# Performance work log

Measured on AMD Instinct MI355X. Metric: run time of the kernel, lower is better.

## Reference

```python
import jax, jax.numpy as jnp
import numpy as np
from math import ceil

EMBED = 512
HEADS = 8
HD = EMBED // HEADS  # 64
FFN = 2048
MIN_CHUNK = 32
LN_EPS = 1e-5


def layer_norm(x, g, b):
    mu = jnp.mean(x, axis=-1, keepdims=True)
    var = jnp.var(x, axis=-1, keepdims=True)
    return (x - mu) * jax.lax.rsqrt(var + LN_EPS) * g + b


def masked_attention(q, k, v, mask_bool, L):
    # q,k,v: [B*H, L, HD]; mask_bool: [B*H, L] (True = padding)
    BH = q.shape[0]
    S = max(MIN_CHUNK, ceil(L / 4))  # dynamic chunk size (static given L)
    C = ceil(L / S)
    pad = C * S - L
    if pad:
        q = jnp.pad(q, ((0, 0), (0, pad), (0, 0)))
        k = jnp.pad(k, ((0, 0), (0, pad), (0, 0)))
        v = jnp.pad(v, ((0, 0), (0, pad), (0, 0)))
        mask_bool = jnp.pad(mask_bool, ((0, 0), (0, pad)), constant_values=True)
    qc = q.reshape(BH, C, S, HD)
    kc = k.reshape(BH, C, S, HD)
    vc = v.reshape(BH, C, S, HD)
    mc = mask_bool.reshape(BH, C, S)
    # pad one phantom (fully masked) chunk on each side, then gather 3-chunk windows
    kp = jnp.pad(kc, ((0, 0), (1, 1), (0, 0), (0, 0)))
    vp = jnp.pad(vc, ((0, 0), (1, 1), (0, 0), (0, 0)))
    mp = jnp.pad(mc, ((0, 0), (1, 1), (0, 0)), constant_values=True)
    k_win = jnp.concatenate([kp[:, i:i + C] for i in range(3)], axis=2)  # [BH,C,3S,HD]
    v_win = jnp.concatenate([vp[:, i:i + C] for i in range(3)], axis=2)
    m_win = jnp.concatenate([mp[:, i:i + C] for i in range(3)], axis=2)  # [BH,C,3S]
    scores = jnp.einsum('bcqd,bckd->bcqk', qc, k_win) / jnp.sqrt(jnp.float32(HD))
    scores = jnp.where(m_win[:, :, None, :], -jnp.inf, scores)
    w = jax.nn.softmax(scores, axis=-1)
    out = jnp.einsum('bcqk,bckd->bcqd', w, v_win)
    return out.reshape(BH, C * S, HD)[:, :L]


def setup_inputs() -> dict:
    key = jax.random.key(0)
    ks = jax.random.split(key, 6)
    B, L, D = 4, 2048, EMBED
    s = 0.02
    return {
        'x': jax.random.normal(ks[0], (B, L, D), jnp.float32),
        'mask': jnp.zeros((B, L), jnp.int32),
        'qkv_w': jax.random.normal(ks[1], (D, 3 * D), jnp.float32) * s,
        'qkv_b': jnp.zeros((3 * D,), jnp.float32),
        'out_w': jax.random.normal(ks[2], (D, D), jnp.float32) * s,
        'out_b': jnp.zeros((D,), jnp.float32),
        'ffn_w1': jax.random.normal(ks[3], (D, FFN), jnp.float32) * s,
        'ffn_b1': jnp.zeros((FFN,), jnp.float32),
        'ffn_w2': jax.random.normal(ks[4], (FFN, D), jnp.float32) * s,
        'ffn_b2': jnp.zeros((D,), jnp.float32),
        'ln1_g': jnp.ones((D,), jnp.float32),
        'ln1_b': jnp.zeros((D,), jnp.float32),
        'ln2_g': jnp.ones((D,), jnp.float32),
        'ln2_b': jnp.zeros((D,), jnp.float32),
    }


def reference(x, mask, qkv_w, qkv_b, out_w, out_b, ffn_w1, ffn_b1, ffn_w2, ffn_b2, ln1_g, ln1_b, ln2_g, ln2_b):
    B, L, D = x.shape
    qkv = x @ qkv_w + qkv_b
    q, k, v = jnp.split(qkv, 3, axis=-1)

    def to_heads(t):
        return t.reshape(B, L, HEADS, HD).transpose(0, 2, 1, 3).reshape(B * HEADS, L, HD)

    mb = jnp.broadcast_to(mask.astype(bool)[:, None, :], (B, HEADS, L)).reshape(B * HEADS, L)
    a = masked_attention(to_heads(q), to_heads(k), to_heads(v), mb, L)
    a = a.reshape(B, HEADS, L, HD).transpose(0, 2, 1, 3).reshape(B, L, D)
    x = x + (a @ out_w + out_b)  # dropout is identity in eval
    x = layer_norm(x, ln1_g, ln1_b)
    h = jax.nn.gelu(x @ ffn_w1 + ffn_b1, approximate=False) @ ffn_w2 + ffn_b2
    x = layer_norm(x + h, ln2_g, ln2_b)
    return x
```

## Files before the change

### kernel.cpp

```cpp
#include <hip/hip_runtime.h>
#include <hip/hip_bf16.h>
#include <math.h>

#define EMBED 512
#define HEADS 8
#define HD    64
#define FFN_  2048
#define NB    4
#define LSEQ  2048
#define MROWS (NB*LSEQ)
#define BHN   (NB*HEADS)

typedef __attribute__((ext_vector_type(8))) short bf16x8;
typedef __attribute__((ext_vector_type(4))) float f32x4;
#define MFMA16(a,b,c) __builtin_amdgcn_mfma_f32_16x16x32_bf16(a,b,c,0,0,0)

__device__ __forceinline__ unsigned short f2bf(float f) {
    unsigned int u = __float_as_uint(f);
    u += 0x7fff + ((u >> 16) & 1);
    return (unsigned short)(u >> 16);
}
__device__ __forceinline__ unsigned int cvt_pk_bf16(float lo, float hi) {
    unsigned int r;
    asm("v_cvt_pk_bf16_f32 %0, %1, %2" : "=v"(r) : "v"(lo), "v"(hi));
    return r;
}
__device__ __forceinline__ void gl_lds16(const unsigned short* g, unsigned short* l) {
    __builtin_amdgcn_global_load_lds(
        (const __attribute__((address_space(1))) unsigned int*)g,
        (__attribute__((address_space(3))) unsigned int*)l, 16, 0, 0);
}
__device__ __forceinline__ float gelu_f(float v) {
    return 0.5f * v * (1.0f + erff(v * 0.70710678118654752f));
}


__global__ __launch_bounds__(256) void cvt_bf16(const float* __restrict__ in,
                                                unsigned short* __restrict__ out, int n) {
    int i = (blockIdx.x * 256 + threadIdx.x) * 8;
    if (i >= n) return;
    float4 a = *reinterpret_cast<const float4*>(&in[i]);
    float4 b = *reinterpret_cast<const float4*>(&in[i + 4]);
    unsigned short t[8] = {f2bf(a.x), f2bf(a.y), f2bf(a.z), f2bf(a.w),
                           f2bf(b.x), f2bf(b.y), f2bf(b.z), f2bf(b.w)};
    *reinterpret_cast<uint4*>(&out[i]) = *reinterpret_cast<uint4*>(t);
}

__global__ __launch_bounds__(256) void wtrans(const float* __restrict__ in,
                                              unsigned short* __restrict__ out,
                                              int K, int N) {
    __shared__ float tile[32][33];
    const int k0 = blockIdx.y * 32, n0 = blockIdx.x * 32;
    const int t = threadIdx.x;
    const int r = t >> 3, c = (t & 7) * 4;
    float4 v = *reinterpret_cast<const float4*>(&in[(size_t)(k0 + r) * N + n0 + c]);
    tile[r][c] = v.x; tile[r][c + 1] = v.y; tile[r][c + 2] = v.z; tile[r][c + 3] = v.w;
    __syncthreads();
    unsigned short tmp[4] = {f2bf(tile[c + 0][r]), f2bf(tile[c + 1][r]),
                             f2bf(tile[c + 2][r]), f2bf(tile[c + 3][r])};
    *reinterpret_cast<uint2*>(&out[(size_t)(n0 + r) * K + k0 + c]) =
        *reinterpret_cast<uint2*>(tmp);
}

__global__ __launch_bounds__(256) void vtransp(const unsigned short* __restrict__ v,
                                               unsigned short* __restrict__ vT) {
    __shared__ unsigned short tile[64][72];
    const int bh = blockIdx.y, l0 = blockIdx.x * 64;
    const int t = threadIdx.x;
    #pragma unroll
    for (int u = 0; u < 2; ++u) {
        int id = t + u * 256; int r = id >> 3, c = (id & 7) * 8;
        *reinterpret_cast<uint4*>(&tile[r][c]) = *reinterpret_cast<const uint4*>(
            &v[((size_t)bh * LSEQ + l0 + r) * HD + c]);
    }
    __syncthreads();
    #pragma unroll
    for (int u = 0; u < 2; ++u) {
        int id = t + u * 256; int d = id >> 3, kc = (id & 7) * 8;
        unsigned short tmp[8];
        #pragma unroll
        for (int jj = 0; jj < 8; ++jj) {
            int kap = kc + jj;
            tmp[jj] = tile[(kap & 3) * 16 + (kap >> 2)][d];
        }
        *reinterpret_cast<uint4*>(&vT[((size_t)bh * HD + d) * LSEQ + l0 + kc]) =
            *reinterpret_cast<uint4*>(tmp);
    }
}

template<int MODE>
__global__ __launch_bounds__(256) void gemm_bf16(
    const unsigned short* __restrict__ A, const unsigned short* __restrict__ WT,
    const float* __restrict__ bias, const float* __restrict__ res,
    void* __restrict__ o0, void* __restrict__ o1, void* __restrict__ o2,
    int M, int N, int K)
{
    __shared__ unsigned short As[128 * 64];
    __shared__ unsigned short Bs[128 * 64];
    const int t = threadIdx.x;
    const int m0 = blockIdx.y * 128, n0 = blockIdx.x * 128;
    const int w = t >> 6, lane = t & 63;
    const int wm = (w >> 1) * 64, wn = (w & 1) * 64;
    const int lr = lane & 15, lk = (lane >> 4) * 8;
    const int rb = (lane >> 4) * 4;
    const int srow = lane >> 3, scol = (lane & 7) * 8;

    f32x4 zero = {0.f, 0.f, 0.f, 0.f};
    f32x4 acc[4][4];
    #pragma unroll
    for (int i = 0; i < 4; ++i)
        #pragma unroll
        for (int j = 0; j < 4; ++j) acc[i][j] = zero;

    for (int k0 = 0; k0 < K; k0 += 64) {
        __syncthreads();
        #pragma unroll
        for (int i = 0; i < 4; ++i) {
            const int seg = w * 4 + i;
            const int r = seg * 8 + srow;
            gl_lds16(A  + (size_t)(m0 + r) * K + k0 + scol, &As[seg * 512 + lane * 8]);
            gl_lds16(WT + (size_t)(n0 + r) * K + k0 + scol, &Bs[seg * 512 + lane * 8]);
        }
        __syncthreads();
        #pragma unroll
        for (int kk = 0; kk < 2; ++kk) {
            bf16x8 a[4], b[4];
            #pragma unroll
            for (int i = 0; i < 4; ++i)
                a[i] = *reinterpret_cast<const bf16x8*>(&As[(wm + i * 16 + lr) * 64 + kk * 32 + lk]);
            #pragma unroll
            for (int j = 0; j < 4; ++j)
                b[j] = *reinterpret_cast<const bf16x8*>(&Bs[(wn + j * 16 + lr) * 64 + kk * 32 + lk]);
            #pragma unroll
            for (int i = 0; i < 4; ++i)
                #pragma unroll
                for (int j = 0; j < 4; ++j)
                    acc[i][j] = MFMA16(a[i], b[j], acc[i][j]);
        }
    }

    #pragma unroll
    for (int i = 0; i < 4; ++i) {
        #pragma unroll
        for (int j = 0; j < 4; ++j) {
            const int n = n0 + wn + j * 16 + lr;
            const float bv = bias[n];
            #pragma unroll
            for (int r = 0; r < 4; ++r) {
                const int m = m0 + wm + i * 16 + rb + r;
                float val = acc[i][j][r] + bv;
                if (MODE == 0) {
                    const int which = n >> 9, nn = n & 511, hs = nn >> 6, d = nn & 63;
                    const int bh = (m >> 11) * 8 + hs, l = m & 2047;
                    unsigned short* p = (which == 0) ? (unsigned short*)o0
                                      : (which == 1) ? (unsigned short*)o1
                                                     : (unsigned short*)o2;
                    p[((size_t)bh * LSEQ + l) * HD + d] = f2bf(val);
                } else {
                    size_t idx = (size_t)m * N + n;
                    ((unsigned short*)o0)[idx] = f2bf(gelu_f(val));
                }
            }
        }
    }
}

__global__ __launch_bounds__(256) void gemm64(
    const unsigned short* __restrict__ A, const unsigned short* __restrict__ WT,
    const float* __restrict__ bias, const float* __restrict__ res,
    float* __restrict__ out, int M, int N, int K)
{
    __shared__ unsigned short As[64 * 64];
    __shared__ unsigned short Bs[64 * 64];
    const int t = threadIdx.x;
    const int m0 = blockIdx.y * 64, n0 = blockIdx.x * 64;
    const int w = t >> 6, lane = t & 63;
    const int wm = (w >> 1) * 32, wn = (w & 1) * 32;
    const int lr = lane & 15, lk = (lane >> 4) * 8;
    const int rb = (lane >> 4) * 4;
    const int srow = t >> 3, scol = (t & 7) * 8;

    f32x4 zero = {0.f, 0.f, 0.f, 0.f};
    f32x4 acc[2][2];
    #pragma unroll
    for (int i = 0; i < 2; ++i)
        #pragma unroll
        for (int j = 0; j < 2; ++j) acc[i][j] = zero;

    for (int k0 = 0; k0 < K; k0 += 64) {
        __syncthreads();
        gl_lds16(A  + (size_t)(m0 + srow)      * K + k0 + scol, &As[t * 8]);
        gl_lds16(A  + (size_t)(m0 + 32 + srow) * K + k0 + scol, &As[2048 + t * 8]);
        gl_lds16(WT + (size_t)(n0 + srow)      * K + k0 + scol, &Bs[t * 8]);
        gl_lds16(WT + (size_t)(n0 + 32 + srow) * K + k0 + scol, &Bs[2048 + t * 8]);
        __syncthreads();
        #pragma unroll
        for (int kk = 0; kk < 2; ++kk) {
            bf16x8 a[2], b[2];
            #pragma unroll
            for (int i = 0; i < 2; ++i)
                a[i] = *reinterpret_cast<const bf16x8*>(&As[(wm + i * 16 + lr) * 64 + kk * 32 + lk]);
            #pragma unroll
            for (int j = 0; j < 2; ++j)
                b[j] = *reinterpret_cast<const bf16x8*>(&Bs[(wn + j * 16 + lr) * 64 + kk * 32 + lk]);
            #pragma unroll
            for (int i = 0; i < 2; ++i)
                #pragma unroll
                for (int j = 0; j < 2; ++j)
                    acc[i][j] = MFMA16(a[i], b[j], acc[i][j]);
        }
    }

    #pragma unroll
    for (int i = 0; i < 2; ++i) {
        #pragma unroll
        for (int j = 0; j < 2; ++j) {
            const int n = n0 + wn + j * 16 + lr;
            const float bv = bias[n];
            #pragma unroll
            for (int r = 0; r < 4; ++r) {
                const int m = m0 + wm + i * 16 + rb + r;
                size_t idx = (size_t)m * N + n;
                out[idx] = acc[i][j][r] + bv + res[idx];
            }
        }
    }
}

__global__ __launch_bounds__(256) void attn_mfma(
    const unsigned short* __restrict__ Q, const unsigned short* __restrict__ K,
    const unsigned short* __restrict__ VTp, const int* __restrict__ mask,
    unsigned short* __restrict__ out)
{
    __shared__ unsigned short Qs[64][72];
    __shared__ unsigned short Ks[64][72];
    __shared__ unsigned short Vs[64][72];
    __shared__ float kbl[64];
    unsigned short (*Ps)[72] = Qs;

    const int bh = blockIdx.x, qt = blockIdx.y;
    const int b = bh >> 3, hh = bh & 7;
    const int t = threadIdx.x, w = t >> 6, lane = t & 63;
    const int lr = lane & 15, lk = (lane >> 4) * 8;
    const int rb = (lane >> 4) * 4;
    const int qr0 = qt * 64;
    const int c = qr0 >> 9;
    const int kstart = max(0, (c - 1) * 512), kend = min(LSEQ, (c + 2) * 512);

    const float C1  = 0.18033688f;
    const float KB0 = -14.4269504f;

    #pragma unroll
    for (int u = 0; u < 2; ++u) {
        int id = t + u * 256; int r = id >> 3, kc = (id & 7) * 8;
        *reinterpret_cast<uint4*>(&Qs[r][kc]) = *reinterpret_cast<const uint4*>(
            &Q[((size_t)bh * LSEQ + qr0 + r) * HD + kc]);
    }
    __syncthreads();
    bf16x8 qf[2];
    qf[0] = *reinterpret_cast<const bf16x8*>(&Qs[w * 16 + lr][lk]);
    qf[1] = *reinterpret_cast<const bf16x8*>(&Qs[w * 16 + lr][32 + lk]);
    bf16x8 vone;
    #pragma unroll
    for (int i = 0; i < 8; ++i) vone[i] = (short)0x3f80;

    f32x4 zero = {0.f, 0.f, 0.f, 0.f};
    f32x4 acc[4], accl = zero;
    #pragma unroll
    for (int j = 0; j < 4; ++j) acc[j] = zero;

    for (int kg = kstart; kg < kend; kg += 64) {
        __syncthreads();
        #pragma unroll
        for (int u = 0; u < 2; ++u) {
            int id = t + u * 256; int r = id >> 3, kc = (id & 7) * 8;
            *reinterpret_cast<uint4*>(&Ks[r][kc]) = *reinterpret_cast<const uint4*>(
                &K[((size_t)bh * LSEQ + kg + r) * HD + kc]);
            *reinterpret_cast<uint4*>(&Vs[r][kc]) = *reinterpret_cast<const uint4*>(
                &VTp[((size_t)bh * HD + r) * LSEQ + kg + kc]);
        }
        if (t < 64) kbl[t] = mask[b * LSEQ + kg + t] ? -1e30f : KB0;
        __syncthreads();

        f32x4 s[4];
        #pragma unroll
        for (int j = 0; j < 4; ++j) s[j] = zero;
        #pragma unroll
        for (int kk = 0; kk < 2; ++kk) {
            #pragma unroll
            for (int j = 0; j < 4; ++j) {
                bf16x8 bk = *reinterpret_cast<const bf16x8*>(&Ks[j * 16 + lr][kk * 32 + lk]);
                s[j] = MFMA16(qf[kk], bk, s[j]);
            }
        }
        #pragma unroll
        for (int r = 0; r < 4; ++r) {
            float p0 = __builtin_amdgcn_exp2f(fmaf(s[0][r], C1, kbl[0 * 16 + lr]));
            float p1 = __builtin_amdgcn_exp2f(fmaf(s[1][r], C1, kbl[1 * 16 + lr]));
            float p2 = __builtin_amdgcn_exp2f(fmaf(s[2][r], C1, kbl[2 * 16 + lr]));
            float p3 = __builtin_amdgcn_exp2f(fmaf(s[3][r], C1, kbl[3 * 16 + lr]));
            uint2 pw;
            pw.x = cvt_pk_bf16(p0, p1);
            pw.y = cvt_pk_bf16(p2, p3);
            *reinterpret_cast<uint2*>(&Ps[w * 16 + rb + r][lr * 4]) = pw;
        }
        #pragma unroll
        for (int kk = 0; kk < 2; ++kk) {
            bf16x8 pa = *reinterpret_cast<const bf16x8*>(&Ps[w * 16 + lr][kk * 32 + lk]);
            #pragma unroll
            for (int j = 0; j < 4; ++j) {
                bf16x8 bv = *reinterpret_cast<const bf16x8*>(&Vs[j * 16 + lr][kk * 32 + lk]);
                acc[j] = MFMA16(pa, bv, acc[j]);
            }
            accl = MFMA16(pa, vone, accl);
        }
    }

    float linv[4];
    #pragma unroll
    for (int r = 0; r < 4; ++r) linv[r] = 1.0f / accl[r];
    #pragma unroll
    for (int j = 0; j < 4; ++j) {
        #pragma unroll
        for (int r = 0; r < 4; ++r) {
            const int l = qr0 + w * 16 + rb + r;
            const int d = j * 16 + lr;
            out[((size_t)(b * LSEQ + l)) * EMBED + hh * HD + d] = f2bf(acc[j][r] * linv[r]);
        }
    }
}

template<int DUAL>
__global__ __launch_bounds__(256) void ln_kernel(
    const float* __restrict__ in, const float* __restrict__ g,
    const float* __restrict__ bt, float* __restrict__ outf,
    unsigned short* __restrict__ outb)
{
    const int row = blockIdx.x;
    const int t = threadIdx.x;
    const float* x = in + (size_t)row * EMBED;
    float2 v = *reinterpret_cast<const float2*>(&x[t * 2]);
    float s = v.x + v.y, ss = v.x * v.x + v.y * v.y;
    #pragma unroll
    for (int off = 1; off < 64; off <<= 1) {
        s  += __shfl_xor(s, off);
        ss += __shfl_xor(ss, off);
    }
    __shared__ float red[8];
    const int w = t >> 6;
    if ((t & 63) == 0) { red[w * 2] = s; red[w * 2 + 1] = ss; }
    __syncthreads();
    s  = red[0] + red[2] + red[4] + red[6];
    ss = red[1] + red[3] + red[5] + red[7];
    const float mu = s * (1.0f / EMBED);
    const float var = ss * (1.0f / EMBED) - mu * mu;
    const float rs = rsqrtf(var + 1e-5f);
    float2 gg = *reinterpret_cast<const float2*>(&g[t * 2]);
    float2 bb = *reinterpret_cast<const float2*>(&bt[t * 2]);
    float ox = (v.x - mu) * rs * gg.x + bb.x;
    float oy = (v.y - mu) * rs * gg.y + bb.y;
    *reinterpret_cast<float2*>(&outf[(size_t)row * EMBED + t * 2]) = make_float2(ox, oy);
    if (DUAL) {
        unsigned short tmp[2] = {f2bf(ox), f2bf(oy)};
        *reinterpret_cast<unsigned int*>(&outb[(size_t)row * EMBED + t * 2]) =
            *reinterpret_cast<unsigned int*>(tmp);
    }
}

extern "C" void kernel_launch(void* const* d_in, const int* in_sizes, int n_in,
                              void* d_out, int out_size, void* d_ws, size_t ws_size,
                              hipStream_t stream) {
    const float* x      = (const float*)d_in[0];
    const int*   mask   = (const int*)  d_in[1];
    const float* qkv_w  = (const float*)d_in[2];
    const float* qkv_b  = (const float*)d_in[3];
    const float* out_w  = (const float*)d_in[4];
    const float* out_b  = (const float*)d_in[5];
    const float* ffn_w1 = (const float*)d_in[6];
    const float* ffn_b1 = (const float*)d_in[7];
    const float* ffn_w2 = (const float*)d_in[8];
    const float* ffn_b2 = (const float*)d_in[9];
    const float* ln1_g  = (const float*)d_in[10];
    const float* ln1_b  = (const float*)d_in[11];
    const float* ln2_g  = (const float*)d_in[12];
    const float* ln2_b  = (const float*)d_in[13];

    char* wsb = (char*)d_ws;
    unsigned short* qkv_wT = (unsigned short*)(wsb + 0);
    unsigned short* out_wT = (unsigned short*)(wsb + 1572864);
    unsigned short* w1T    = (unsigned short*)(wsb + 2097152);
    unsigned short* w2T    = (unsigned short*)(wsb + 4194304);
    unsigned short* xb     = (unsigned short*)(wsb + 6291456);
    unsigned short* qb     = (unsigned short*)(wsb + 14680064);
    unsigned short* kbuf   = (unsigned short*)(wsb + 23068672);
    unsigned short* vb     = (unsigned short*)(wsb + 31457280);
    float*          y      = (float*)(wsb + 39845888);
    unsigned short* vTp    = xb;
    unsigned short* am     = vb;
    unsigned short* xlnb   = xb;
    float*          xlnf   = (float*)(wsb + 14680064);
    unsigned short* h      = (unsigned short*)(wsb + 31457280);
    float*          z      = (float*)(wsb + 65011712);

    cvt_bf16<<<MROWS * EMBED / 8 / 256, 256, 0, stream>>>(x, xb, MROWS * EMBED);
    wtrans<<<dim3(1536 / 32, 512 / 32),  256, 0, stream>>>(qkv_w,  qkv_wT, 512, 1536);
    wtrans<<<dim3(512 / 32,  512 / 32),  256, 0, stream>>>(out_w,  out_wT, 512, 512);
    wtrans<<<dim3(2048 / 32, 512 / 32),  256, 0, stream>>>(ffn_w1, w1T,    512, 2048);
    wtrans<<<dim3(512 / 32,  2048 / 32), 256, 0, stream>>>(ffn_w2, w2T,    2048, 512);

    gemm_bf16<0><<<dim3(1536 / 128, MROWS / 128), 256, 0, stream>>>(
        xb, qkv_wT, qkv_b, nullptr, qb, kbuf, vb, MROWS, 1536, 512);
    vtransp<<<dim3(LSEQ / 64, BHN), 256, 0, stream>>>(vb, vTp);
    attn_mfma<<<dim3(BHN, LSEQ / 64), 256, 0, stream>>>(qb, kbuf, vTp, mask, am);
    gemm64<<<dim3(EMBED / 64, MROWS / 64), 256, 0, stream>>>(
        am, out_wT, out_b, x, y, MROWS, EMBED, 512);
    ln_kernel<1><<<MROWS, 256, 0, stream>>>(y, ln1_g, ln1_b, xlnf, xlnb);
    gemm_bf16<2><<<dim3(FFN_ / 128, MROWS / 128), 256, 0, stream>>>(
        xlnb, w1T, ffn_b1, nullptr, h, nullptr, nullptr, MROWS, FFN_, 512);
    gemm64<<<dim3(EMBED / 64, MROWS / 64), 256, 0, stream>>>(
        h, w2T, ffn_b2, xlnf, z, MROWS, EMBED, FFN_);
    ln_kernel<0><<<MROWS, 256, 0, stream>>>(z, ln2_g, ln2_b, (float*)d_out, nullptr);
}
```

Baseline: 296.1 us.

## Rework attention tiling, GELU, LayerNorm, and precision with XCD block swizzle

The attention kernel now handles 128 query rows per block: Q fragments load straight from global memory, and row sums come from a register accumulation plus a shuffle reduction instead of an extra MFMA against a ones vector. GELU switches from exact erf to a tanh approximation built on exp2 and rcp. LayerNorm kernels now use one wave per row with no shared-memory reduction. The LN1 input and residual are held in bf16 instead of fp32, and GEMM blocks are remapped to spread work across XCDs. These changes cut memory traffic and instruction count, at the cost of reduced numerical precision from bf16 residuals and the approximate GELU.

```diff
diff --git a/kernel.cpp b/kernel.cpp
--- a/kernel.cpp
+++ b/kernel.cpp
@@ -20,6 +20,9 @@
     u += 0x7fff + ((u >> 16) & 1);
     return (unsigned short)(u >> 16);
 }
+__device__ __forceinline__ float bf2f(unsigned short u) {
+    return __uint_as_float(((unsigned int)u) << 16);
+}
 __device__ __forceinline__ unsigned int cvt_pk_bf16(float lo, float hi) {
     unsigned int r;
     asm("v_cvt_pk_bf16_f32 %0, %1, %2" : "=v"(r) : "v"(lo), "v"(hi));
@@ -30,8 +33,19 @@
         (const __attribute__((address_space(1))) unsigned int*)g,
         (__attribute__((address_space(3))) unsigned int*)l, 16, 0, 0);
 }
-__device__ __forceinline__ float gelu_f(float v) {
-    return 0.5f * v * (1.0f + erff(v * 0.70710678118654752f));
+__device__ __forceinline__ float gelu_f(float x) {
+    float u = x * fmaf(x * x, 0.044715f, 1.0f) * 0.7978845608f;
+    float a = fminf(fmaxf(u * 2.885390082f, -30.f), 30.f);
+    float t = __builtin_amdgcn_exp2f(a);
+    return x * t * __builtin_amdgcn_rcpf(t + 1.0f);
+}
+__device__ __forceinline__ void xcd_swz(int& bx, int& by, int gx, int gy) {
+    int nwg = gx * gy;
+    int lid = by * gx + bx;
+    int cpx = nwg >> 3;
+    int swz = (lid & 7) * cpx + (lid >> 3);
+    bx = swz % gx;
+    by = swz / gx;
 }
 
 
@@ -91,14 +105,16 @@
 template<int MODE>
 __global__ __launch_bounds__(256) void gemm_bf16(
     const unsigned short* __restrict__ A, const unsigned short* __restrict__ WT,
-    const float* __restrict__ bias, const float* __restrict__ res,
+    const float* __restrict__ bias,
     void* __restrict__ o0, void* __restrict__ o1, void* __restrict__ o2,
     int M, int N, int K)
 {
     __shared__ unsigned short As[128 * 64];
     __shared__ unsigned short Bs[128 * 64];
+    int bx = blockIdx.x, by = blockIdx.y;
+    xcd_swz(bx, by, gridDim.x, gridDim.y);
     const int t = threadIdx.x;
-    const int m0 = blockIdx.y * 128, n0 = blockIdx.x * 128;
+    const int m0 = by * 128, n0 = bx * 128;
     const int w = t >> 6, lane = t & 63;
     const int wm = (w >> 1) * 64, wn = (w & 1) * 64;
     const int lr = lane & 15, lk = (lane >> 4) * 8;
@@ -165,15 +181,18 @@
     }
 }
 
+template<int MODE>
 __global__ __launch_bounds__(256) void gemm64(
     const unsigned short* __restrict__ A, const unsigned short* __restrict__ WT,
-    const float* __restrict__ bias, const float* __restrict__ res,
-    float* __restrict__ out, int M, int N, int K)
+    const float* __restrict__ bias, const void* __restrict__ res,
+    void* __restrict__ out, int M, int N, int K)
 {
     __shared__ unsigned short As[64 * 64];
     __shared__ unsigned short Bs[64 * 64];
+    int bx = blockIdx.x, by = blockIdx.y;
+    xcd_swz(bx, by, gridDim.x, gridDim.y);
     const int t = threadIdx.x;
-    const int m0 = blockIdx.y * 64, n0 = blockIdx.x * 64;
+    const int m0 = by * 64, n0 = bx * 64;
     const int w = t >> 6, lane = t & 63;
     const int wm = (w >> 1) * 32, wn = (w & 1) * 32;
     const int lr = lane & 15, lk = (lane >> 4) * 8;
@@ -221,7 +240,14 @@
             for (int r = 0; r < 4; ++r) {
                 const int m = m0 + wm + i * 16 + rb + r;
                 size_t idx = (size_t)m * N + n;
-                out[idx] = acc[i][j][r] + bv + res[idx];
+                float val = acc[i][j][r] + bv;
+                if (MODE == 0) {
+                    val += ((const float*)res)[idx];
+                    ((unsigned short*)out)[idx] = f2bf(val);
+                } else {
+                    val += bf2f(((const unsigned short*)res)[idx]);
+                    ((float*)out)[idx] = val;
+                }
             }
         }
     }
@@ -232,42 +258,43 @@
     const unsigned short* __restrict__ VTp, const int* __restrict__ mask,
     unsigned short* __restrict__ out)
 {
-    __shared__ unsigned short Qs[64][72];
     __shared__ unsigned short Ks[64][72];
     __shared__ unsigned short Vs[64][72];
+    __shared__ unsigned short Ps[128][72];
     __shared__ float kbl[64];
-    unsigned short (*Ps)[72] = Qs;
-
-    const int bh = blockIdx.x, qt = blockIdx.y;
+
+    int bx = blockIdx.x, by = blockIdx.y;
+    xcd_swz(bx, by, 16, 32);
+    const int qt = bx, bh = by;
     const int b = bh >> 3, hh = bh & 7;
     const int t = threadIdx.x, w = t >> 6, lane = t & 63;
-    const int lr = lane & 15, lk = (lane >> 4) * 8;
-    const int rb = (lane >> 4) * 4;
-    const int qr0 = qt * 64;
+    const int lr = lane & 15, hi = lane >> 4;
+    const int lk = hi * 8, rb = hi * 4;
+    const int qr0 = qt * 128;
     const int c = qr0 >> 9;
     const int kstart = max(0, (c - 1) * 512), kend = min(LSEQ, (c + 2) * 512);
 
     const float C1  = 0.18033688f;
     const float KB0 = -14.4269504f;
 
-    #pragma unroll
-    for (int u = 0; u < 2; ++u) {
-        int id = t + u * 256; int r = id >> 3, kc = (id & 7) * 8;
-        *reinterpret_cast<uint4*>(&Qs[r][kc]) = *reinterpret_cast<const uint4*>(
-            &Q[((size_t)bh * LSEQ + qr0 + r) * HD + kc]);
-    }
-    __syncthreads();
-    bf16x8 qf[2];
-    qf[0] = *reinterpret_cast<const bf16x8*>(&Qs[w * 16 + lr][lk]);
-    qf[1] = *reinterpret_cast<const bf16x8*>(&Qs[w * 16 + lr][32 + lk]);
-    bf16x8 vone;
-    #pragma unroll
-    for (int i = 0; i < 8; ++i) vone[i] = (short)0x3f80;
+    bf16x8 qf[2][2];
+    #pragma unroll
+    for (int fi = 0; fi < 2; ++fi)
+        #pragma unroll
+        for (int kk = 0; kk < 2; ++kk)
+            qf[fi][kk] = *reinterpret_cast<const bf16x8*>(
+                &Q[((size_t)bh * LSEQ + qr0 + w * 32 + fi * 16 + lr) * HD + kk * 32 + lk]);
 
     f32x4 zero = {0.f, 0.f, 0.f, 0.f};
-    f32x4 acc[4], accl = zero;
-    #pragma unroll
-    for (int j = 0; j < 4; ++j) acc[j] = zero;
+    f32x4 acc[2][4];
+    float lsum[2][4];
+    #pragma unroll
+    for (int fi = 0; fi < 2; ++fi) {
+        #pragma unroll
+        for (int j = 0; j < 4; ++j) acc[fi][j] = zero;
+        #pragma unroll
+        for (int r = 0; r < 4; ++r) lsum[fi][r] = 0.f;
+    }
 
     for (int kg = kstart; kg < kend; kg += 64) {
         __syncthreads();
@@ -282,89 +309,144 @@
         if (t < 64) kbl[t] = mask[b * LSEQ + kg + t] ? -1e30f : KB0;
         __syncthreads();
 
-        f32x4 s[4];
-        #pragma unroll
-        for (int j = 0; j < 4; ++j) s[j] = zero;
+        f32x4 s[2][4];
+        #pragma unroll
+        for (int fi = 0; fi < 2; ++fi)
+            #pragma unroll
+            for (int j = 0; j < 4; ++j) s[fi][j] = zero;
         #pragma unroll
         for (int kk = 0; kk < 2; ++kk) {
             #pragma unroll
             for (int j = 0; j < 4; ++j) {
                 bf16x8 bk = *reinterpret_cast<const bf16x8*>(&Ks[j * 16 + lr][kk * 32 + lk]);
-                s[j] = MFMA16(qf[kk], bk, s[j]);
+                s[0][j] = MFMA16(qf[0][kk], bk, s[0][j]);
+                s[1][j] = MFMA16(qf[1][kk], bk, s[1][j]);
             }
         }
         #pragma unroll
-        for (int r = 0; r < 4; ++r) {
-            float p0 = __builtin_amdgcn_exp2f(fmaf(s[0][r], C1, kbl[0 * 16 + lr]));
-            float p1 = __builtin_amdgcn_exp2f(fmaf(s[1][r], C1, kbl[1 * 16 + lr]));
-            float p2 = __builtin_amdgcn_exp2f(fmaf(s[2][r], C1, kbl[2 * 16 + lr]));
-            float p3 = __builtin_amdgcn_exp2f(fmaf(s[3][r], C1, kbl[3 * 16 + lr]));
-            uint2 pw;
-            pw.x = cvt_pk_bf16(p0, p1);
-            pw.y = cvt_pk_bf16(p2, p3);
-            *reinterpret_cast<uint2*>(&Ps[w * 16 + rb + r][lr * 4]) = pw;
+        for (int fi = 0; fi < 2; ++fi) {
+            #pragma unroll
+            for (int r = 0; r < 4; ++r) {
+                float p0 = __builtin_amdgcn_exp2f(fmaf(s[fi][0][r], C1, kbl[0 * 16 + lr]));
+                float p1 = __builtin_amdgcn_exp2f(fmaf(s[fi][1][r], C1, kbl[1 * 16 + lr]));
+                float p2 = __builtin_amdgcn_exp2f(fmaf(s[fi][2][r], C1, kbl[2 * 16 + lr]));
+                float p3 = __builtin_amdgcn_exp2f(fmaf(s[fi][3][r], C1, kbl[3 * 16 + lr]));
+                lsum[fi][r] += (p0 + p1) + (p2 + p3);
+                uint2 pw;
+                pw.x = cvt_pk_bf16(p0, p1);
+                pw.y = cvt_pk_bf16(p2, p3);
+                *reinterpret_cast<uint2*>(&Ps[w * 32 + fi * 16 + rb + r][lr * 4]) = pw;
+            }
         }
         #pragma unroll
         for (int kk = 0; kk < 2; ++kk) {
-            bf16x8 pa = *reinterpret_cast<const bf16x8*>(&Ps[w * 16 + lr][kk * 32 + lk]);
+            bf16x8 pa0 = *reinterpret_cast<const bf16x8*>(&Ps[w * 32 + lr][kk * 32 + lk]);
+            bf16x8 pa1 = *reinterpret_cast<const bf16x8*>(&Ps[w * 32 + 16 + lr][kk * 32 + lk]);
             #pragma unroll
             for (int j = 0; j < 4; ++j) {
                 bf16x8 bv = *reinterpret_cast<const bf16x8*>(&Vs[j * 16 + lr][kk * 32 + lk]);
-                acc[j] = MFMA16(pa, bv, acc[j]);
+                acc[0][j] = MFMA16(pa0, bv, acc[0][j]);
+                acc[1][j] = MFMA16(pa1, bv, acc[1][j]);
             }
-            accl = MFMA16(pa, vone, accl);
-        }
-    }
-
-    float linv[4];
-    #pragma unroll
-    for (int r = 0; r < 4; ++r) linv[r] = 1.0f / accl[r];
-    #pragma unroll
-    for (int j = 0; j < 4; ++j) {
+        }
+    }
+
+    float linv[2][4];
+    #pragma unroll
+    for (int fi = 0; fi < 2; ++fi)
         #pragma unroll
         for (int r = 0; r < 4; ++r) {
-            const int l = qr0 + w * 16 + rb + r;
-            const int d = j * 16 + lr;
-            out[((size_t)(b * LSEQ + l)) * EMBED + hh * HD + d] = f2bf(acc[j][r] * linv[r]);
-        }
-    }
-}
-
-template<int DUAL>
-__global__ __launch_bounds__(256) void ln_kernel(
-    const float* __restrict__ in, const float* __restrict__ g,
-    const float* __restrict__ bt, float* __restrict__ outf,
-    unsigned short* __restrict__ outb)
+            float v = lsum[fi][r];
+            v += __shfl_xor(v, 1, 16);
+            v += __shfl_xor(v, 2, 16);
+            v += __shfl_xor(v, 4, 16);
+            v += __shfl_xor(v, 8, 16);
+            linv[fi][r] = 1.0f / v;
+        }
+    #pragma unroll
+    for (int fi = 0; fi < 2; ++fi)
+        #pragma unroll
+        for (int j = 0; j < 4; ++j)
+            #pragma unroll
+            for (int r = 0; r < 4; ++r) {
+                const int l = qr0 + w * 32 + fi * 16 + rb + r;
+                const int d = j * 16 + lr;
+                out[((size_t)(b * LSEQ + l)) * EMBED + hh * HD + d] =
+                    f2bf(acc[fi][j][r] * linv[fi][r]);
+            }
+}
+
+__global__ __launch_bounds__(256) void ln_b2b(
+    const unsigned short* __restrict__ in, const float* __restrict__ g,
+    const float* __restrict__ bt, unsigned short* __restrict__ out)
 {
-    const int row = blockIdx.x;
-    const int t = threadIdx.x;
-    const float* x = in + (size_t)row * EMBED;
-    float2 v = *reinterpret_cast<const float2*>(&x[t * 2]);
-    float s = v.x + v.y, ss = v.x * v.x + v.y * v.y;
+    const int t = threadIdx.x, lane = t & 63;
+    const int row = blockIdx.x * 4 + (t >> 6);
+    uint4 raw = *reinterpret_cast<const uint4*>(&in[(size_t)row * EMBED + lane * 8]);
+    float v[8];
+    const unsigned int* rw = reinterpret_cast<const unsigned int*>(&raw);
+    #pragma unroll
+    for (int i = 0; i < 4; ++i) {
+        v[2 * i]     = __uint_as_float(rw[i] << 16);
+        v[2 * i + 1] = __uint_as_float(rw[i] & 0xffff0000u);
+    }
+    float s = 0.f, ss = 0.f;
+    #pragma unroll
+    for (int i = 0; i < 8; ++i) { s += v[i]; ss += v[i] * v[i]; }
     #pragma unroll
     for (int off = 1; off < 64; off <<= 1) {
         s  += __shfl_xor(s, off);
         ss += __shfl_xor(ss, off);
     }
-    __shared__ float red[8];
-    const int w = t >> 6;
-    if ((t & 63) == 0) { red[w * 2] = s; red[w * 2 + 1] = ss; }
-    __syncthreads();
-    s  = red[0] + red[2] + red[4] + red[6];
-    ss = red[1] + red[3] + red[5] + red[7];
     const float mu = s * (1.0f / EMBED);
     const float var = ss * (1.0f / EMBED) - mu * mu;
     const float rs = rsqrtf(var + 1e-5f);
-    float2 gg = *reinterpret_cast<const float2*>(&g[t * 2]);
-    float2 bb = *reinterpret_cast<const float2*>(&bt[t * 2]);
-    float ox = (v.x - mu) * rs * gg.x + bb.x;
-    float oy = (v.y - mu) * rs * gg.y + bb.y;
-    *reinterpret_cast<float2*>(&outf[(size_t)row * EMBED + t * 2]) = make_float2(ox, oy);
-    if (DUAL) {
-        unsigned short tmp[2] = {f2bf(ox), f2bf(oy)};
-        *reinterpret_cast<unsigned int*>(&outb[(size_t)row * EMBED + t * 2]) =
-            *reinterpret_cast<unsigned int*>(tmp);
-    }
+    float4 g0 = *reinterpret_cast<const float4*>(&g[lane * 8]);
+    float4 g1 = *reinterpret_cast<const float4*>(&g[lane * 8 + 4]);
+    float4 b0 = *reinterpret_cast<const float4*>(&bt[lane * 8]);
+    float4 b1 = *reinterpret_cast<const float4*>(&bt[lane * 8 + 4]);
+    float gg[8] = {g0.x, g0.y, g0.z, g0.w, g1.x, g1.y, g1.z, g1.w};
+    float bb[8] = {b0.x, b0.y, b0.z, b0.w, b1.x, b1.y, b1.z, b1.w};
+    unsigned short o[8];
+    #pragma unroll
+    for (int i = 0; i < 8; ++i) o[i] = f2bf((v[i] - mu) * rs * gg[i] + bb[i]);
+    *reinterpret_cast<uint4*>(&out[(size_t)row * EMBED + lane * 8]) =
+        *reinterpret_cast<uint4*>(o);
+}
+
+__global__ __launch_bounds__(256) void ln_f2f(
+    const float* __restrict__ in, const float* __restrict__ g,
+    const float* __restrict__ bt, float* __restrict__ out)
+{
+    const int t = threadIdx.x, lane = t & 63;
+    const int row = blockIdx.x * 4 + (t >> 6);
+    const float* x = in + (size_t)row * EMBED + lane * 8;
+    float4 a = *reinterpret_cast<const float4*>(x);
+    float4 b2 = *reinterpret_cast<const float4*>(x + 4);
+    float v[8] = {a.x, a.y, a.z, a.w, b2.x, b2.y, b2.z, b2.w};
+    float s = 0.f, ss = 0.f;
+    #pragma unroll
+    for (int i = 0; i < 8; ++i) { s += v[i]; ss += v[i] * v[i]; }
+    #pragma unroll
+    for (int off = 1; off < 64; off <<= 1) {
+        s  += __shfl_xor(s, off);
+        ss += __shfl_xor(ss, off);
+    }
+    const float mu = s * (1.0f / EMBED);
+    const float var = ss * (1.0f / EMBED) - mu * mu;
+    const float rs = rsqrtf(var + 1e-5f);
+    float4 g0 = *reinterpret_cast<const float4*>(&g[lane * 8]);
+    float4 g1 = *reinterpret_cast<const float4*>(&g[lane * 8 + 4]);
+    float4 b0 = *reinterpret_cast<const float4*>(&bt[lane * 8]);
+    float4 b1 = *reinterpret_cast<const float4*>(&bt[lane * 8 + 4]);
+    float gg[8] = {g0.x, g0.y, g0.z, g0.w, g1.x, g1.y, g1.z, g1.w};
+    float bb[8] = {b0.x, b0.y, b0.z, b0.w, b1.x, b1.y, b1.z, b1.w};
+    float o[8];
+    #pragma unroll
+    for (int i = 0; i < 8; ++i) o[i] = (v[i] - mu) * rs * gg[i] + bb[i];
+    float* op = out + (size_t)row * EMBED + lane * 8;
+    *reinterpret_cast<float4*>(op)     = make_float4(o[0], o[1], o[2], o[3]);
+    *reinterpret_cast<float4*>(op + 4) = make_float4(o[4], o[5], o[6], o[7]);
 }
 
 extern "C" void kernel_launch(void* const* d_in, const int* in_sizes, int n_in,
@@ -394,11 +476,10 @@
     unsigned short* qb     = (unsigned short*)(wsb + 14680064);
     unsigned short* kbuf   = (unsigned short*)(wsb + 23068672);
     unsigned short* vb     = (unsigned short*)(wsb + 31457280);
-    float*          y      = (float*)(wsb + 39845888);
+    unsigned short* y      = (unsigned short*)(wsb + 39845888);
     unsigned short* vTp    = xb;
     unsigned short* am     = vb;
     unsigned short* xlnb   = xb;
-    float*          xlnf   = (float*)(wsb + 14680064);
     unsigned short* h      = (unsigned short*)(wsb + 31457280);
     float*          z      = (float*)(wsb + 65011712);
 
@@ -409,15 +490,15 @@
     wtrans<<<dim3(512 / 32,  2048 / 32), 256, 0, stream>>>(ffn_w2, w2T,    2048, 512);
 
     gemm_bf16<0><<<dim3(1536 / 128, MROWS / 128), 256, 0, stream>>>(
-        xb, qkv_wT, qkv_b, nullptr, qb, kbuf, vb, MROWS, 1536, 512);
+        xb, qkv_wT, qkv_b, qb, kbuf, vb, MROWS, 1536, 512);
     vtransp<<<dim3(LSEQ / 64, BHN), 256, 0, stream>>>(vb, vTp);
-    attn_mfma<<<dim3(BHN, LSEQ / 64), 256, 0, stream>>>(qb, kbuf, vTp, mask, am);
-    gemm64<<<dim3(EMBED / 64, MROWS / 64), 256, 0, stream>>>(
+    attn_mfma<<<dim3(LSEQ / 128, BHN), 256, 0, stream>>>(qb, kbuf, vTp, mask, am);
+    gemm64<0><<<dim3(EMBED / 64, MROWS / 64), 256, 0, stream>>>(
         am, out_wT, out_b, x, y, MROWS, EMBED, 512);
-    ln_kernel<1><<<MROWS, 256, 0, stream>>>(y, ln1_g, ln1_b, xlnf, xlnb);
+    ln_b2b<<<MROWS / 4, 256, 0, stream>>>(y, ln1_g, ln1_b, xlnb);
     gemm_bf16<2><<<dim3(FFN_ / 128, MROWS / 128), 256, 0, stream>>>(
-        xlnb, w1T, ffn_b1, nullptr, h, nullptr, nullptr, MROWS, FFN_, 512);
-    gemm64<<<dim3(EMBED / 64, MROWS / 64), 256, 0, stream>>>(
-        h, w2T, ffn_b2, xlnf, z, MROWS, EMBED, FFN_);
-    ln_kernel<0><<<MROWS, 256, 0, stream>>>(z, ln2_g, ln2_b, (float*)d_out, nullptr);
-}
+        xlnb, w1T, ffn_b1, h, nullptr, nullptr, MROWS, FFN_, 512);
+    gemm64<1><<<dim3(EMBED / 64, MROWS / 64), 256, 0, stream>>>(
+        h, w2T, ffn_b2, xlnb, z, MROWS, EMBED, FFN_);
+    ln_f2f<<<MROWS / 4, 256, 0, stream>>>(z, ln2_g, ln2_b, (float*)d_out);
+}
```

Result: faster. 286.1 us (-3.4%).
